# Performance work log

Hardware: AMD Instinct MI355X
Metric: run time of the kernel (lower is better)

Reference implementation:

```python
import jax, jax.numpy as jnp
import numpy as np

# --- configuration (mirrors init_kwargs) ---
N_G = (256, 256, 128, 128)   # tem.hyper['n_g'] per-module sizes
N_ACTIONS = 4                 # tem action space
NUM_STATES = 4096
BATCH = 16384
G_TOTAL = sum(N_G)            # 768


def setup_inputs() -> dict:
    key = jax.random.key(0)
    ks = jax.random.split(key, 4 + len(N_G))
    inp = {
        "current_state_index": jax.random.randint(ks[0], (BATCH,), 0, NUM_STATES),
        "action_index": jax.random.randint(ks[1], (BATCH,), 0, N_ACTIONS),
        # xavier-ish init scale for embedding / classifier
        "emb": jax.random.normal(ks[2], (NUM_STATES, G_TOTAL), jnp.float32) * 0.02,
        "W_cls": jax.random.normal(ks[3], (NUM_STATES, G_TOTAL), jnp.float32) * 0.02,
        "b_cls": jnp.zeros((NUM_STATES,), jnp.float32),
    }
    # per-module bank of action-conditioned transition matrices D_a: [n_actions, n_g_f, n_g_f]
    for f, n in enumerate(N_G):
        inp[f"D{f}"] = jax.random.normal(ks[4 + f], (N_ACTIONS, n, n), jnp.float32) * (1.0 / np.sqrt(n))
    return inp


def _transition(g_f, D_f, onehot):
    # Routed action-conditioned transition (replaces the CPU per-action loop):
    # delta[b, j] = sum_i D_f[a_b, j, i] * g_f[b, i], dispatched via one-hot over actions.
    delta = jnp.einsum('aji,bi,ba->bj', D_f, g_f, onehot)
    # TEM generative clamp activation f_g_clamp
    return jnp.clip(g_f + delta, -1.0, 1.0)


def reference(current_state_index, action_index, emb, D0, D1, D2, D3, W_cls, b_cls):
    g_flat = emb[current_state_index]                                   # [B, G_TOTAL]
    onehot = jax.nn.one_hot(action_index, N_ACTIONS, dtype=g_flat.dtype)  # [B, A]
    # _split_g: slice flat grid code into TEM modules
    g_mods = jnp.split(g_flat, np.cumsum(np.array(N_G))[:-1].tolist(), axis=1)
    Ds = (D0, D1, D2, D3)
    g_next = [_transition(g_f, D_f, onehot) for g_f, D_f in zip(g_mods, Ds)]
    g_next_flat = jnp.concatenate(g_next, axis=1)                       # [B, G_TOTAL]
    logits = g_next_flat @ W_cls.T + b_cls                              # [B, NUM_STATES]
    return logits, g_next_flat
```

## Files before the change

kernel.cpp:

```cpp
#include <hip/hip_runtime.h>
#include <hip/hip_bf16.h>
#include <stdint.h>


typedef __attribute__((ext_vector_type(8))) short short8;
typedef __attribute__((ext_vector_type(4))) float floatx4;

__device__ __forceinline__ float bf2f(short s) {
    unsigned int u = ((unsigned int)(unsigned short)s) << 16;
    float f;
    __builtin_memcpy(&f, &u, 4);
    return f;
}
__device__ __forceinline__ short f2bf(float f) {
    unsigned int u;
    __builtin_memcpy(&u, &f, 4);
    u = (u + 0x7FFFu + ((u >> 16) & 1u)) >> 16;
    return (short)u;
}

#define GLLDS16(g, l)                                                                     \
    __builtin_amdgcn_global_load_lds((const __attribute__((address_space(1))) void*)(g),  \
                                     (__attribute__((address_space(3))) void*)(l), 16, 0, 0)

__global__ __launch_bounds__(256) void prep_kernel(
    const int* __restrict__ state, const float* __restrict__ emb,
    const float* __restrict__ W, const float* __restrict__ D0,
    const float* __restrict__ D1, const float* __restrict__ D2,
    const float* __restrict__ D3, short* __restrict__ A1,
    short* __restrict__ Wb, short* __restrict__ Db) {
    long e = (long)blockIdx.x * 256 + threadIdx.x;
    const float* src;
    short* dst;
    long di;
    if (e < 3145728L) {
        int b = (int)(e / 192);
        int cc = (int)(e % 192);
        int s = state[b];
        src = emb + (long)s * 768 + cc * 4;
        dst = A1; di = e;
    } else if (e < 3932160L) {
        long t = e - 3145728L;
        src = W + t * 4; dst = Wb; di = t;
    } else if (e < 3997696L) {
        long t = e - 3932160L;
        src = D0 + t * 4; dst = Db; di = t;
    } else if (e < 4063232L) {
        long t = e - 3997696L;
        src = D1 + t * 4; dst = Db + 262144; di = t;
    } else if (e < 4079616L) {
        long t = e - 4063232L;
        src = D2 + t * 4; dst = Db + 524288; di = t;
    } else {
        long t = e - 4079616L;
        src = D3 + t * 4; dst = Db + 589824; di = t;
    }
    float4 v = *(const float4*)src;
    union { ushort4 u4; short s4[4]; } o;
    o.s4[0] = f2bf(v.x); o.s4[1] = f2bf(v.y);
    o.s4[2] = f2bf(v.z); o.s4[3] = f2bf(v.w);
    *(ushort4*)(dst + di * 4) = o.u4;
}

__global__ __launch_bounds__(256) void trans_gemm_kernel(
    const short* __restrict__ A, const short* __restrict__ Bm,
    const int* __restrict__ act, float* __restrict__ gnext,
    short* __restrict__ A2, int n, int K) {
    __shared__ short Ash[128 * 64];
    __shared__ short Bsh[128 * 64];
    const int tid = threadIdx.x;
    const int lane = tid & 63;
    const int w = tid >> 6;
    const int wm = w & 1, wn = w >> 1;
    const int bn = blockIdx.x, bm = blockIdx.y;
    const long arow0 = (long)bm * 128;
    const long brow0 = (long)bn * 128;
    const int lrow = lane & 15;
    const int q = lane >> 4;

    floatx4 acc[4][4] = {};

    for (int k0 = 0; k0 < K; k0 += 64) {
        #pragma unroll
        for (int it = 0; it < 4; ++it) {
            int c = it * 256 + tid;
            int r = c >> 3, cc = c & 7;
            int gc = cc ^ (r & 7);
            GLLDS16(A + (arow0 + r) * 768 + k0 + gc * 8, &Ash[c * 8]);
            GLLDS16(Bm + (brow0 + r) * (long)n + k0 + gc * 8, &Bsh[c * 8]);
        }
        __syncthreads();
        #pragma unroll
        for (int kk = 0; kk < 2; ++kk) {
            short8 af[4], bv[4];
            #pragma unroll
            for (int mi = 0; mi < 4; ++mi) {
                int rr = wm * 64 + mi * 16 + lrow;
                int ch = (kk * 4 + q) ^ (rr & 7);
                af[mi] = *(const short8*)&Ash[rr * 64 + ch * 8];
            }
            #pragma unroll
            for (int ni = 0; ni < 4; ++ni) {
                int rr = wn * 64 + ni * 16 + lrow;
                int ch = (kk * 4 + q) ^ (rr & 7);
                bv[ni] = *(const short8*)&Bsh[rr * 64 + ch * 8];
            }
            #pragma unroll
            for (int mi = 0; mi < 4; ++mi)
                #pragma unroll
                for (int ni = 0; ni < 4; ++ni)
                    acc[mi][ni] = __builtin_amdgcn_mfma_f32_16x16x32_bf16(
                        af[mi], bv[ni], acc[mi][ni], 0, 0, 0);
        }
        __syncthreads();
    }

    const int tile_action = (bn * 128) / n;
    const int jb = bn * 128 - tile_action * n + wn * 64;
    const int rowbase = bm * 128 + wm * 64;
    #pragma unroll
    for (int mi = 0; mi < 4; ++mi) {
        #pragma unroll
        for (int r = 0; r < 4; ++r) {
            int row = rowbase + mi * 16 + q * 4 + r;
            if (act[row] == tile_action) {
                #pragma unroll
                for (int ni = 0; ni < 4; ++ni) {
                    int jl = jb + ni * 16 + lrow;
                    long idx = (long)row * 768 + jl;
                    float g = bf2f(A[idx]);
                    float v = g + acc[mi][ni][r];
                    v = fminf(1.0f, fmaxf(-1.0f, v));
                    gnext[idx] = v;
                    A2[idx] = f2bf(v);
                }
            }
        }
    }
}

__global__ __launch_bounds__(256) void cls_gemm_kernel(
    const short* __restrict__ A, const short* __restrict__ Bm,
    const float* __restrict__ bias, float* __restrict__ out) {
    __shared__ short Ash[128 * 64];
    __shared__ short Bsh[128 * 64];
    const int tid = threadIdx.x;
    const int lane = tid & 63;
    const int w = tid >> 6;
    const int wm = w & 1, wn = w >> 1;
    const int bn = blockIdx.x, bm = blockIdx.y;
    const long arow0 = (long)bm * 128;
    const long brow0 = (long)bn * 128;
    const int lrow = lane & 15;
    const int q = lane >> 4;

    floatx4 acc[4][4] = {};

    for (int k0 = 0; k0 < 768; k0 += 64) {
        #pragma unroll
        for (int it = 0; it < 4; ++it) {
            int c = it * 256 + tid;
            int r = c >> 3, cc = c & 7;
            int gc = cc ^ (r & 7);
            GLLDS16(A + (arow0 + r) * 768 + k0 + gc * 8, &Ash[c * 8]);
            GLLDS16(Bm + (brow0 + r) * 768 + k0 + gc * 8, &Bsh[c * 8]);
        }
        __syncthreads();
        #pragma unroll
        for (int kk = 0; kk < 2; ++kk) {
            short8 af[4], bv[4];
            #pragma unroll
            for (int mi = 0; mi < 4; ++mi) {
                int rr = wm * 64 + mi * 16 + lrow;
                int ch = (kk * 4 + q) ^ (rr & 7);
                af[mi] = *(const short8*)&Ash[rr * 64 + ch * 8];
            }
            #pragma unroll
            for (int ni = 0; ni < 4; ++ni) {
                int rr = wn * 64 + ni * 16 + lrow;
                int ch = (kk * 4 + q) ^ (rr & 7);
                bv[ni] = *(const short8*)&Bsh[rr * 64 + ch * 8];
            }
            #pragma unroll
            for (int mi = 0; mi < 4; ++mi)
                #pragma unroll
                for (int ni = 0; ni < 4; ++ni)
                    acc[mi][ni] = __builtin_amdgcn_mfma_f32_16x16x32_bf16(
                        af[mi], bv[ni], acc[mi][ni], 0, 0, 0);
        }
        __syncthreads();
    }

    const int rowbase = bm * 128 + wm * 64;
    const int colbase = bn * 128 + wn * 64;
    #pragma unroll
    for (int mi = 0; mi < 4; ++mi) {
        #pragma unroll
        for (int r = 0; r < 4; ++r) {
            int row = rowbase + mi * 16 + q * 4 + r;
            #pragma unroll
            for (int ni = 0; ni < 4; ++ni) {
                int col = colbase + ni * 16 + lrow;
                out[(long)row * 4096 + col] = acc[mi][ni][r] + bias[col];
            }
        }
    }
}

extern "C" void kernel_launch(void* const* d_in, const int* in_sizes, int n_in,
                              void* d_out, int out_size, void* d_ws, size_t ws_size,
                              hipStream_t stream) {
    const int* state  = (const int*)d_in[0];
    const int* act    = (const int*)d_in[1];
    const float* emb  = (const float*)d_in[2];
    const float* W    = (const float*)d_in[3];
    const float* bias = (const float*)d_in[4];
    const float* D0   = (const float*)d_in[5];
    const float* D1   = (const float*)d_in[6];
    const float* D2   = (const float*)d_in[7];
    const float* D3   = (const float*)d_in[8];

    float* logits = (float*)d_out;
    float* gnext  = logits + 67108864L;

    short* A1 = (short*)d_ws;
    short* A2 = A1 + 12582912L;
    short* Wb = A2 + 12582912L;
    short* Db = Wb + 3145728L;

    prep_kernel<<<16000, 256, 0, stream>>>(state, emb, W, D0, D1, D2, D3, A1, Wb, Db);

    trans_gemm_kernel<<<dim3(8, 128), 256, 0, stream>>>(A1, Db, act, gnext, A2, 256, 256);
    trans_gemm_kernel<<<dim3(8, 128), 256, 0, stream>>>(A1 + 256, Db + 262144, act,
                                                        gnext + 256, A2 + 256, 256, 256);
    trans_gemm_kernel<<<dim3(4, 128), 256, 0, stream>>>(A1 + 512, Db + 524288, act,
                                                        gnext + 512, A2 + 512, 128, 128);
    trans_gemm_kernel<<<dim3(4, 128), 256, 0, stream>>>(A1 + 640, Db + 589824, act,
                                                        gnext + 640, A2 + 640, 128, 128);

    cls_gemm_kernel<<<dim3(32, 128), 256, 0, stream>>>(A2, Wb, bias, logits);
}
```

Measured before the change: 541.4 us.

## Group batch rows by action and run one routed transition GEMM

Rows are bucketed by action through count, scan and scatter kernels. A single grouped transition GEMM then gathers each action's rows and multiplies them only by that action's D matrix, instead of computing all four actions for every row and masking the results. The four per-module launches are also merged into one grid. The cost is three extra small kernels, atomics, and gathered (non-contiguous) row loads.

```diff
diff --git a/kernel.cpp b/kernel.cpp
--- a/kernel.cpp
+++ b/kernel.cpp
@@ -23,12 +23,14 @@
     __builtin_amdgcn_global_load_lds((const __attribute__((address_space(1))) void*)(g),  \
                                      (__attribute__((address_space(3))) void*)(l), 16, 0, 0)
 
+
 __global__ __launch_bounds__(256) void prep_kernel(
     const int* __restrict__ state, const float* __restrict__ emb,
     const float* __restrict__ W, const float* __restrict__ D0,
     const float* __restrict__ D1, const float* __restrict__ D2,
     const float* __restrict__ D3, short* __restrict__ A1,
-    short* __restrict__ Wb, short* __restrict__ Db) {
+    short* __restrict__ Wb, short* __restrict__ Db, int* __restrict__ meta) {
+    if (blockIdx.x == 0 && threadIdx.x < 4) meta[threadIdx.x] = 0;
     long e = (long)blockIdx.x * 256 + threadIdx.x;
     const float* src;
     short* dst;
@@ -62,32 +64,87 @@
     *(ushort4*)(dst + di * 4) = o.u4;
 }
 
+__global__ __launch_bounds__(256) void count_kernel(const int* __restrict__ act,
+                                                    int* __restrict__ meta) {
+    __shared__ int lc[4];
+    if (threadIdx.x < 4) lc[threadIdx.x] = 0;
+    __syncthreads();
+    int i = blockIdx.x * 256 + threadIdx.x;
+    atomicAdd(&lc[act[i]], 1);
+    __syncthreads();
+    if (threadIdx.x < 4) atomicAdd(&meta[threadIdx.x], lc[threadIdx.x]);
+}
+
+__global__ void scan_kernel(int* __restrict__ meta) {
+    if (threadIdx.x == 0) {
+        int o = 0, t = 0;
+        meta[8] = 0;
+        for (int a = 0; a < 4; ++a) {
+            meta[4 + a] = o;
+            meta[13 + a] = o;
+            o += meta[a];
+            t += (meta[a] + 127) >> 7;
+            meta[9 + a] = t;
+        }
+    }
+}
+
+__global__ __launch_bounds__(256) void scatter_kernel(const int* __restrict__ act,
+                                                      int* __restrict__ meta,
+                                                      int* __restrict__ rowidx) {
+    int i = blockIdx.x * 256 + threadIdx.x;
+    int a = act[i];
+    int slot = atomicAdd(&meta[13 + a], 1);
+    rowidx[slot] = i;
+}
+
 __global__ __launch_bounds__(256) void trans_gemm_kernel(
-    const short* __restrict__ A, const short* __restrict__ Bm,
-    const int* __restrict__ act, float* __restrict__ gnext,
-    short* __restrict__ A2, int n, int K) {
+    const short* __restrict__ A1, const short* __restrict__ Db,
+    const int* __restrict__ meta, const int* __restrict__ rowidx,
+    float* __restrict__ gnext, short* __restrict__ A2) {
     __shared__ short Ash[128 * 64];
     __shared__ short Bsh[128 * 64];
+    __shared__ int ridx[128];
+    const int ty = blockIdx.y;
+    if (ty >= meta[12]) return;
+    int a = 0;
+    #pragma unroll
+    for (int i = 1; i < 4; ++i)
+        if (ty >= meta[8 + i]) a = i;
+    const int rtile = ty - meta[8 + a];
+    const int cnt   = meta[a];
+    const int off   = meta[4 + a];
+    const int cval  = min(128, cnt - rtile * 128);
+
+    const int slot = blockIdx.x;
+    const int mod  = slot < 4 ? (slot >> 1) : slot - 2;
+    const int colt = slot < 4 ? (slot & 1) : 0;
+    const int n    = mod < 2 ? 256 : 128;
+    const int aoff = mod < 2 ? mod * 256 : 512 + (mod - 2) * 128;
+    const long doff = mod == 0 ? 0L : mod == 1 ? 262144L : mod == 2 ? 524288L : 589824L;
+    const short* Bm = Db + doff + ((long)a * n + colt * 128) * n;
+
     const int tid = threadIdx.x;
+    if (tid < 128) ridx[tid] = rowidx[off + rtile * 128 + min(tid, cval - 1)];
+    __syncthreads();
+
     const int lane = tid & 63;
     const int w = tid >> 6;
     const int wm = w & 1, wn = w >> 1;
-    const int bn = blockIdx.x, bm = blockIdx.y;
-    const long arow0 = (long)bm * 128;
-    const long brow0 = (long)bn * 128;
     const int lrow = lane & 15;
     const int q = lane >> 4;
 
     floatx4 acc[4][4] = {};
 
-    for (int k0 = 0; k0 < K; k0 += 64) {
+    for (int k0 = 0; k0 < n; k0 += 64) {
         #pragma unroll
         for (int it = 0; it < 4; ++it) {
             int c = it * 256 + tid;
             int r = c >> 3, cc = c & 7;
             int gc = cc ^ (r & 7);
-            GLLDS16(A + (arow0 + r) * 768 + k0 + gc * 8, &Ash[c * 8]);
-            GLLDS16(Bm + (brow0 + r) * (long)n + k0 + gc * 8, &Bsh[c * 8]);
+            int row = ridx[r];
+            GLLDS16(A1 + (long)row * 768 + aoff + k0 + gc * 8, &Ash[c * 8]);
+            GLLDS16(Bm + (long)r * n + k0 + gc * 8, &Bsh[c * 8]);
         }
         __syncthreads();
         #pragma unroll
@@ -115,21 +172,20 @@
         __syncthreads();
     }
 
-    const int tile_action = (bn * 128) / n;
-    const int jb = bn * 128 - tile_action * n + wn * 64;
-    const int rowbase = bm * 128 + wm * 64;
+    const int jb = colt * 128 + wn * 64;
     #pragma unroll
     for (int mi = 0; mi < 4; ++mi) {
         #pragma unroll
-        for (int r = 0; r < 4; ++r) {
-            int row = rowbase + mi * 16 + q * 4 + r;
-            if (act[row] == tile_action) {
+        for (int r4 = 0; r4 < 4; ++r4) {
+            int local = wm * 64 + mi * 16 + q * 4 + r4;
+            if (local < cval) {
+                int row = ridx[local];
                 #pragma unroll
                 for (int ni = 0; ni < 4; ++ni) {
                     int jl = jb + ni * 16 + lrow;
-                    long idx = (long)row * 768 + jl;
-                    float g = bf2f(A[idx]);
-                    float v = g + acc[mi][ni][r];
+                    long idx = (long)row * 768 + aoff + jl;
+                    float g = bf2f(A1[idx]);
+                    float v = g + acc[mi][ni][r4];
                     v = fminf(1.0f, fmaxf(-1.0f, v));
                     gnext[idx] = v;
                     A2[idx] = f2bf(v);
@@ -227,16 +283,13 @@
     short* A2 = A1 + 12582912L;
     short* Wb = A2 + 12582912L;
     short* Db = Wb + 3145728L;
-
-    prep_kernel<<<16000, 256, 0, stream>>>(state, emb, W, D0, D1, D2, D3, A1, Wb, Db);
-
-    trans_gemm_kernel<<<dim3(8, 128), 256, 0, stream>>>(A1, Db, act, gnext, A2, 256, 256);
-    trans_gemm_kernel<<<dim3(8, 128), 256, 0, stream>>>(A1 + 256, Db + 262144, act,
-                                                        gnext + 256, A2 + 256, 256, 256);
-    trans_gemm_kernel<<<dim3(4, 128), 256, 0, stream>>>(A1 + 512, Db + 524288, act,
-                                                        gnext + 512, A2 + 512, 128, 128);
-    trans_gemm_kernel<<<dim3(4, 128), 256, 0, stream>>>(A1 + 640, Db + 589824, act,
-                                                        gnext + 640, A2 + 640, 128, 128);
-
+    int*   meta   = (int*)(Db + 655360);
+    int*   rowidx = meta + 32;
+
+    prep_kernel<<<16000, 256, 0, stream>>>(state, emb, W, D0, D1, D2, D3, A1, Wb, Db, meta);
+    count_kernel<<<64, 256, 0, stream>>>(act, meta);
+    scan_kernel<<<1, 64, 0, stream>>>(meta);
+    scatter_kernel<<<64, 256, 0, stream>>>(act, meta, rowidx);
+    trans_gemm_kernel<<<dim3(6, 131), 256, 0, stream>>>(A1, Db, meta, rowidx, gnext, A2);
     cls_gemm_kernel<<<dim3(32, 128), 256, 0, stream>>>(A2, Wb, bias, logits);
 }
```

After: 571.5 us. +5.6%, slower.
